# Performance work log

Measured on AMD Instinct MI355X. Metric: run time of the kernel, lower is better.

Reference implementation:

```python
import jax, jax.numpy as jnp
import numpy as np

N = 100000
NCLASS = 64
E = 1600000
NHID = 256
TOPK = 16
DEGREE = 9


def setup_inputs() -> dict:
    key = jax.random.key(0)
    ks = jax.random.split(key, 10)
    return {
        "f_prediction": jax.random.normal(ks[0], (N, NCLASS), dtype=jnp.float32),
        "g0_prediction": jax.random.normal(ks[1], (N, NCLASS), dtype=jnp.float32),
        "adj_rows": jax.random.randint(ks[2], (E,), 0, N, dtype=jnp.int32),
        "adj_cols": jax.random.randint(ks[3], (E,), 0, N, dtype=jnp.int32),
        "adj_vals": jax.random.uniform(ks[4], (E,), dtype=jnp.float32) / 16.0,
        "W1": jax.random.normal(ks[5], (TOPK, 2 * NHID), dtype=jnp.float32) * 0.1,
        "b1": jnp.zeros((2 * NHID,), dtype=jnp.float32),
        "W2": jax.random.normal(ks[6], (2 * NHID, NHID), dtype=jnp.float32) * 0.1,
        "b2": jnp.zeros((NHID,), dtype=jnp.float32),
        "W3": jax.random.normal(ks[7], (NHID, DEGREE), dtype=jnp.float32) * 0.1,
        "b3": jnp.zeros((DEGREE,), dtype=jnp.float32),
    }


def spmm(rows, cols, vals, x):
    # out[i] = sum_{e: rows[e]==i} vals[e] * x[cols[e]]
    msgs = vals[:, None] * x[cols]  # [E, F]
    return jax.ops.segment_sum(msgs, rows, num_segments=N)


def reference(f_prediction, g0_prediction, adj_rows, adj_cols, adj_vals,
              W1, b1, W2, b2, W3, b3):
    g0 = jax.nn.softmax(g0_prediction, axis=1)
    ranked, _ = jax.lax.top_k(g0, TOPK)  # [N, TOPK], sorted descending
    h = jnp.tanh(ranked @ W1 + b1)
    h = jnp.tanh(h @ W2 + b2)
    weight = h @ W3 + b3  # [N, DEGREE]

    f = f_prediction
    final = weight[:, 0:1] * f
    for i in range(DEGREE - 1):
        f = spmm(adj_rows, adj_cols, adj_vals, f)
        final = final + weight[:, i + 1:i + 2] * f
    return jax.nn.log_softmax(final, axis=1), weight
```

## Files before the change

### kernel.cpp

```cpp
#include <hip/hip_runtime.h>
#include <hip/hip_bf16.h>

#define N_NODES 100000
#define NCLASS  64
#define NEDGE   1600000
#define NHID    256
#define TOPK    16
#define DEGREE  9

#define TM 16
#define KCHUNK 128
#define H2PAD (NHID + 4)

__device__ __forceinline__ float fast_tanh(float x) {
    float e = __expf(2.0f * x);
    return 1.0f - 2.0f / (e + 1.0f);
}


__global__ void hist_kernel(const int* __restrict__ rows, int* __restrict__ counts, int e) {
    for (int i = blockIdx.x * blockDim.x + threadIdx.x; i < e; i += gridDim.x * blockDim.x)
        atomicAdd(&counts[rows[i]], 1);
}

__global__ __launch_bounds__(1024) void scan_blocks(const int* __restrict__ counts,
                                                    int* __restrict__ partial,
                                                    int* __restrict__ blocksums, int n) {
    __shared__ int s[1024];
    int tid = threadIdx.x;
    int gid = blockIdx.x * 1024 + tid;
    int v = (gid < n) ? counts[gid] : 0;
    s[tid] = v;
    __syncthreads();
    for (int off = 1; off < 1024; off <<= 1) {
        int t = (tid >= off) ? s[tid - off] : 0;
        __syncthreads();
        s[tid] += t;
        __syncthreads();
    }
    if (gid < n) partial[gid] = s[tid] - v;
    if (tid == 1023) blocksums[blockIdx.x] = s[1023];
}

__global__ void scan_sums(int* __restrict__ blocksums, int nb) {
    if (blockIdx.x == 0 && threadIdx.x == 0) {
        int run = 0;
        for (int i = 0; i < nb; ++i) { int v = blocksums[i]; blocksums[i] = run; run += v; }
    }
}

__global__ void finalize_rows(const int* __restrict__ partial, const int* __restrict__ blocksums,
                              int* __restrict__ row_start, int* __restrict__ cursor, int n, int e) {
    int i = blockIdx.x * blockDim.x + threadIdx.x;
    if (i < n) {
        int v = partial[i] + blocksums[i >> 10];
        row_start[i] = v;
        cursor[i] = v;
    }
    if (i == 0) row_start[n] = e;
}

__global__ void scatter_edges(const int* __restrict__ rows, const int* __restrict__ cols,
                              const float* __restrict__ vals, int* __restrict__ cursor,
                              int2* __restrict__ sedge, int e) {
    for (int i = blockIdx.x * blockDim.x + threadIdx.x; i < e; i += gridDim.x * blockDim.x) {
        int r = rows[i];
        int pos = atomicAdd(&cursor[r], 1);
        sedge[pos] = make_int2(cols[i], __float_as_int(vals[i]));
    }
}


__global__ __launch_bounds__(256) void softmax_topk(const float* __restrict__ g0,
                                                    float* __restrict__ ranked, int n) {
    int wave = (blockIdx.x * 256 + threadIdx.x) >> 6;
    int lane = threadIdx.x & 63;
    if (wave >= n) return;
    float x = g0[(size_t)wave * NCLASS + lane];
    float m = x;
    #pragma unroll
    for (int o = 1; o < 64; o <<= 1) m = fmaxf(m, __shfl_xor(m, o));
    float p = expf(x - m);
    float s = p;
    #pragma unroll
    for (int o = 1; o < 64; o <<= 1) s += __shfl_xor(s, o);
    p /= s;
    float v = p;
    #pragma unroll
    for (int k = 2; k <= 64; k <<= 1) {
        #pragma unroll
        for (int j = k >> 1; j > 0; j >>= 1) {
            float o = __shfl_xor(v, j);
            bool up = (lane & k) != 0;
            bool takeMax = (((lane & j) == 0) != up);
            v = takeMax ? fmaxf(v, o) : fminf(v, o);
        }
    }
    if (lane < TOPK) ranked[wave * TOPK + lane] = v;
}


__global__ __launch_bounds__(256) void mlp_kernel(const float* __restrict__ ranked,
                                                  const float* __restrict__ W1, const float* __restrict__ b1,
                                                  const float* __restrict__ W2, const float* __restrict__ b2,
                                                  const float* __restrict__ W3, const float* __restrict__ b3,
                                                  float* __restrict__ weight_out, int n) {
    __shared__ float s_rank[TM][TOPK];
    __shared__ float s_h1[TM][KCHUNK];
    __shared__ float s_h2[TM][H2PAD];
    int t = threadIdx.x;
    int row0 = blockIdx.x * TM;

    {
        int r = t >> 4, k = t & 15;
        int gr = row0 + r;
        s_rank[r][k] = (gr < n) ? ranked[gr * TOPK + k] : 0.0f;
    }

    const int tx = t & 63;
    const int ty = t >> 6;
    float acc[4][4];
    {
        float4 b2v = *reinterpret_cast<const float4*>(&b2[tx * 4]);
        #pragma unroll
        for (int rr = 0; rr < 4; ++rr) {
            acc[rr][0] = b2v.x; acc[rr][1] = b2v.y; acc[rr][2] = b2v.z; acc[rr][3] = b2v.w;
        }
    }
    const float* w2p = W2 + tx * 4;

    const int j  = t & (KCHUNK - 1);
    const int rh = (t >> 7) * 8;

    __syncthreads();

    for (int c = 0; c < 2 * NHID / KCHUNK; ++c) {
        const int kbase = c * KCHUNK;
        {
            const int col = kbase + j;
            float w1c[TOPK];
            #pragma unroll
            for (int k = 0; k < TOPK; ++k) w1c[k] = W1[k * (2 * NHID) + col];
            float bb = b1[col];
            #pragma unroll
            for (int r = rh; r < rh + 8; ++r) {
                float4 q0 = *reinterpret_cast<const float4*>(&s_rank[r][0]);
                float4 q1 = *reinterpret_cast<const float4*>(&s_rank[r][4]);
                float4 q2 = *reinterpret_cast<const float4*>(&s_rank[r][8]);
                float4 q3 = *reinterpret_cast<const float4*>(&s_rank[r][12]);
                float rk[TOPK] = {q0.x, q0.y, q0.z, q0.w, q1.x, q1.y, q1.z, q1.w,
                                  q2.x, q2.y, q2.z, q2.w, q3.x, q3.y, q3.z, q3.w};
                float a = bb;
                #pragma unroll
                for (int k = 0; k < TOPK; ++k) a = fmaf(rk[k], w1c[k], a);
                s_h1[r][j] = fast_tanh(a);
            }
        }
        __syncthreads();

        for (int kk = 0; kk < KCHUNK; kk += 4) {
            float4 h[4];
            #pragma unroll
            for (int rr = 0; rr < 4; ++rr)
                h[rr] = *reinterpret_cast<const float4*>(&s_h1[ty * 4 + rr][kk]);
            #pragma unroll
            for (int kk2 = 0; kk2 < 4; ++kk2) {
                float4 w = *reinterpret_cast<const float4*>(&w2p[(size_t)(kbase + kk + kk2) * NHID]);
                #pragma unroll
                for (int rr = 0; rr < 4; ++rr) {
                    float hv = (kk2 == 0) ? h[rr].x : (kk2 == 1) ? h[rr].y : (kk2 == 2) ? h[rr].z : h[rr].w;
                    acc[rr][0] = fmaf(hv, w.x, acc[rr][0]);
                    acc[rr][1] = fmaf(hv, w.y, acc[rr][1]);
                    acc[rr][2] = fmaf(hv, w.z, acc[rr][2]);
                    acc[rr][3] = fmaf(hv, w.w, acc[rr][3]);
                }
            }
        }
        __syncthreads();
    }

    #pragma unroll
    for (int rr = 0; rr < 4; ++rr) {
        #pragma unroll
        for (int cc = 0; cc < 4; ++cc)
            s_h2[ty * 4 + rr][tx * 4 + cc] = fast_tanh(acc[rr][cc]);
    }
    __syncthreads();

    if (t < TM * DEGREE) {
        int r = t / DEGREE, d = t % DEGREE;
        float a3 = b3[d];
        for (int k = 0; k < NHID; k += 4) {
            float4 h = *reinterpret_cast<const float4*>(&s_h2[r][k]);
            a3 = fmaf(h.x, W3[(k + 0) * DEGREE + d], a3);
            a3 = fmaf(h.y, W3[(k + 1) * DEGREE + d], a3);
            a3 = fmaf(h.z, W3[(k + 2) * DEGREE + d], a3);
            a3 = fmaf(h.w, W3[(k + 3) * DEGREE + d], a3);
        }
        int gr = row0 + r;
        if (gr < n) weight_out[gr * DEGREE + d] = a3;
    }
}


__global__ void init_final(const float* __restrict__ fpred, const float* __restrict__ weight,
                           float* __restrict__ finalbuf, int n) {
    int i = blockIdx.x * blockDim.x + threadIdx.x;
    if (i < n * NCLASS) {
        int row = i >> 6;
        finalbuf[i] = weight[row * DEGREE] * fpred[i];
    }
}

__global__ __launch_bounds__(256) void spmm_fused(const int* __restrict__ row_start,
                                                  const int2* __restrict__ sedge,
                                                  const float* __restrict__ x,
                                                  float* __restrict__ y,
                                                  const float* __restrict__ weight,
                                                  float* __restrict__ finalbuf,
                                                  int wcol, int n) {
    int wave = (blockIdx.x * 256 + threadIdx.x) >> 6;
    int lane = threadIdx.x & 63;
    if (wave >= n) return;
    int e0 = row_start[wave], e1 = row_start[wave + 1];
    float a0 = 0.0f, a1 = 0.0f, a2 = 0.0f, a3 = 0.0f;
    int e = e0;
    for (; e + 3 < e1; e += 4) {
        int2 d0 = sedge[e];
        int2 d1 = sedge[e + 1];
        int2 d2 = sedge[e + 2];
        int2 d3 = sedge[e + 3];
        float x0 = x[(size_t)d0.x * NCLASS + lane];
        float x1 = x[(size_t)d1.x * NCLASS + lane];
        float x2 = x[(size_t)d2.x * NCLASS + lane];
        float x3 = x[(size_t)d3.x * NCLASS + lane];
        a0 = fmaf(__int_as_float(d0.y), x0, a0);
        a1 = fmaf(__int_as_float(d1.y), x1, a1);
        a2 = fmaf(__int_as_float(d2.y), x2, a2);
        a3 = fmaf(__int_as_float(d3.y), x3, a3);
    }
    for (; e < e1; ++e) {
        int2 d = sedge[e];
        a0 = fmaf(__int_as_float(d.y), x[(size_t)d.x * NCLASS + lane], a0);
    }
    float acc = (a0 + a1) + (a2 + a3);
    int o = wave * NCLASS + lane;
    y[o] = acc;
    finalbuf[o] += weight[wave * DEGREE + wcol] * acc;
}

__global__ __launch_bounds__(256) void logsoftmax_inplace(float* __restrict__ out, int n) {
    int wave = (blockIdx.x * 256 + threadIdx.x) >> 6;
    int lane = threadIdx.x & 63;
    if (wave >= n) return;
    int o = wave * NCLASS + lane;
    float x = out[o];
    float m = x;
    #pragma unroll
    for (int off = 1; off < 64; off <<= 1) m = fmaxf(m, __shfl_xor(m, off));
    float p = expf(x - m);
    float s = p;
    #pragma unroll
    for (int off = 1; off < 64; off <<= 1) s += __shfl_xor(s, off);
    out[o] = x - m - logf(s);
}


extern "C" void kernel_launch(void* const* d_in, const int* in_sizes, int n_in,
                              void* d_out, int out_size, void* d_ws, size_t ws_size,
                              hipStream_t stream) {
    const float* f_pred = (const float*)d_in[0];
    const float* g0     = (const float*)d_in[1];
    const int*   arows  = (const int*)d_in[2];
    const int*   acols  = (const int*)d_in[3];
    const float* avals  = (const float*)d_in[4];
    const float* W1     = (const float*)d_in[5];
    const float* b1     = (const float*)d_in[6];
    const float* W2     = (const float*)d_in[7];
    const float* b2     = (const float*)d_in[8];
    const float* W3     = (const float*)d_in[9];
    const float* b3     = (const float*)d_in[10];

    float* out_ls = (float*)d_out;
    float* weight = (float*)d_out + (size_t)N_NODES * NCLASS;

    char* ws = (char*)d_ws;
    size_t off = 0;
    auto alloc = [&](size_t bytes) {
        void* p = ws + off;
        off += (bytes + 255) & ~(size_t)255;
        return p;
    };
    float* ranked    = (float*)alloc((size_t)N_NODES * TOPK * 4);
    float* fA        = (float*)alloc((size_t)N_NODES * NCLASS * 4);
    float* fB        = (float*)alloc((size_t)N_NODES * NCLASS * 4);
    int*   counts    = (int*)alloc((size_t)N_NODES * 4);
    int*   partial   = (int*)alloc((size_t)N_NODES * 4);
    int*   row_start = (int*)alloc((size_t)(N_NODES + 1) * 4);
    int*   cursor    = (int*)alloc((size_t)N_NODES * 4);
    int*   blocksums = (int*)alloc(128 * 4);
    int2*  sedge     = (int2*)alloc((size_t)NEDGE * 8);

    const int SCAN_BLOCKS = (N_NODES + 1023) / 1024;

    hipMemsetAsync(counts, 0, (size_t)N_NODES * 4, stream);
    hist_kernel<<<2048, 256, 0, stream>>>(arows, counts, NEDGE);
    scan_blocks<<<SCAN_BLOCKS, 1024, 0, stream>>>(counts, partial, blocksums, N_NODES);
    scan_sums<<<1, 64, 0, stream>>>(blocksums, SCAN_BLOCKS);
    finalize_rows<<<(N_NODES + 255) / 256, 256, 0, stream>>>(partial, blocksums, row_start, cursor,
                                                             N_NODES, NEDGE);
    scatter_edges<<<2048, 256, 0, stream>>>(arows, acols, avals, cursor, sedge, NEDGE);

    softmax_topk<<<(N_NODES + 3) / 4, 256, 0, stream>>>(g0, ranked, N_NODES);
    mlp_kernel<<<(N_NODES + TM - 1) / TM, 256, 0, stream>>>(ranked, W1, b1, W2, b2, W3, b3,
                                                            weight, N_NODES);

    init_final<<<(N_NODES * NCLASS + 255) / 256, 256, 0, stream>>>(f_pred, weight, out_ls, N_NODES);

    const float* xin = f_pred;
    float* bufs[2] = {fA, fB};
    for (int it = 0; it < DEGREE - 1; ++it) {
        float* y = bufs[it & 1];
        spmm_fused<<<(N_NODES + 3) / 4, 256, 0, stream>>>(row_start, sedge, xin, y, weight, out_ls,
                                                          it + 1, N_NODES);
        xin = y;
    }

    logsoftmax_inplace<<<(N_NODES + 3) / 4, 256, 0, stream>>>(out_ls, N_NODES);
}
```

Before: 1.516 ms.

## Enlarge MLP row tile, prefetch W2 rows, and unroll SpMM gather by eight

Result: faster. 1.377 ms (-9.2%).

```diff
diff --git a/kernel.cpp b/kernel.cpp
--- a/kernel.cpp
+++ b/kernel.cpp
@@ -8,7 +8,7 @@
 #define TOPK    16
 #define DEGREE  9
 
-#define TM 16
+#define TM 32
 #define KCHUNK 128
 #define H2PAD (NHID + 4)
 
@@ -111,26 +111,25 @@
     int t = threadIdx.x;
     int row0 = blockIdx.x * TM;
 
-    {
-        int r = t >> 4, k = t & 15;
+    for (int idx = t; idx < TM * TOPK; idx += 256) {
+        int r = idx >> 4, k = idx & 15;
         int gr = row0 + r;
         s_rank[r][k] = (gr < n) ? ranked[gr * TOPK + k] : 0.0f;
     }
 
     const int tx = t & 63;
     const int ty = t >> 6;
-    float acc[4][4];
+    float acc[8][4];
     {
         float4 b2v = *reinterpret_cast<const float4*>(&b2[tx * 4]);
         #pragma unroll
-        for (int rr = 0; rr < 4; ++rr) {
+        for (int rr = 0; rr < 8; ++rr) {
             acc[rr][0] = b2v.x; acc[rr][1] = b2v.y; acc[rr][2] = b2v.z; acc[rr][3] = b2v.w;
         }
     }
-    const float* w2p = W2 + tx * 4;
 
     const int j  = t & (KCHUNK - 1);
-    const int rh = (t >> 7) * 8;
+    const int rh = (t >> 7) * (TM / 2);
 
     __syncthreads();
 
@@ -142,8 +141,8 @@
             #pragma unroll
             for (int k = 0; k < TOPK; ++k) w1c[k] = W1[k * (2 * NHID) + col];
             float bb = b1[col];
-            #pragma unroll
-            for (int r = rh; r < rh + 8; ++r) {
+            #pragma unroll 4
+            for (int r = rh; r < rh + TM / 2; ++r) {
                 float4 q0 = *reinterpret_cast<const float4*>(&s_rank[r][0]);
                 float4 q1 = *reinterpret_cast<const float4*>(&s_rank[r][4]);
                 float4 q2 = *reinterpret_cast<const float4*>(&s_rank[r][8]);
@@ -158,21 +157,38 @@
         }
         __syncthreads();
 
-        for (int kk = 0; kk < KCHUNK; kk += 4) {
-            float4 h[4];
-            #pragma unroll
-            for (int rr = 0; rr < 4; ++rr)
-                h[rr] = *reinterpret_cast<const float4*>(&s_h1[ty * 4 + rr][kk]);
-            #pragma unroll
-            for (int kk2 = 0; kk2 < 4; ++kk2) {
-                float4 w = *reinterpret_cast<const float4*>(&w2p[(size_t)(kbase + kk + kk2) * NHID]);
+        {
+            const float* wk = W2 + (size_t)kbase * NHID + (tx << 2);
+            float4 wa0 = *reinterpret_cast<const float4*>(wk);
+            float4 wa1 = *reinterpret_cast<const float4*>(wk + NHID);
+            float4 wa2 = *reinterpret_cast<const float4*>(wk + 2 * NHID);
+            float4 wa3 = *reinterpret_cast<const float4*>(wk + 3 * NHID);
+            wk += 4 * NHID;
+            for (int kk = 0; kk < KCHUNK; kk += 4) {
+                float4 w0 = wa0, w1 = wa1, w2v = wa2, w3v = wa3;
+                if (kk + 4 < KCHUNK) {
+                    wa0 = *reinterpret_cast<const float4*>(wk);
+                    wa1 = *reinterpret_cast<const float4*>(wk + NHID);
+                    wa2 = *reinterpret_cast<const float4*>(wk + 2 * NHID);
+                    wa3 = *reinterpret_cast<const float4*>(wk + 3 * NHID);
+                    wk += 4 * NHID;
+                }
+                float4 h[8];
                 #pragma unroll
-                for (int rr = 0; rr < 4; ++rr) {
-                    float hv = (kk2 == 0) ? h[rr].x : (kk2 == 1) ? h[rr].y : (kk2 == 2) ? h[rr].z : h[rr].w;
-                    acc[rr][0] = fmaf(hv, w.x, acc[rr][0]);
-                    acc[rr][1] = fmaf(hv, w.y, acc[rr][1]);
-                    acc[rr][2] = fmaf(hv, w.z, acc[rr][2]);
-                    acc[rr][3] = fmaf(hv, w.w, acc[rr][3]);
+                for (int rr = 0; rr < 8; ++rr)
+                    h[rr] = *reinterpret_cast<const float4*>(&s_h1[ty * 8 + rr][kk]);
+                #pragma unroll
+                for (int kk2 = 0; kk2 < 4; ++kk2) {
+                    float4 w = (kk2 == 0) ? w0 : (kk2 == 1) ? w1 : (kk2 == 2) ? w2v : w3v;
+                    #pragma unroll
+                    for (int rr = 0; rr < 8; ++rr) {
+                        float hv = (kk2 == 0) ? h[rr].x : (kk2 == 1) ? h[rr].y
+                                 : (kk2 == 2) ? h[rr].z : h[rr].w;
+                        acc[rr][0] = fmaf(hv, w.x, acc[rr][0]);
+                        acc[rr][1] = fmaf(hv, w.y, acc[rr][1]);
+                        acc[rr][2] = fmaf(hv, w.z, acc[rr][2]);
+                        acc[rr][3] = fmaf(hv, w.w, acc[rr][3]);
+                    }
                 }
             }
         }
@@ -180,15 +196,15 @@
     }
 
     #pragma unroll
-    for (int rr = 0; rr < 4; ++rr) {
+    for (int rr = 0; rr < 8; ++rr) {
         #pragma unroll
         for (int cc = 0; cc < 4; ++cc)
-            s_h2[ty * 4 + rr][tx * 4 + cc] = fast_tanh(acc[rr][cc]);
+            s_h2[ty * 8 + rr][tx * 4 + cc] = fast_tanh(acc[rr][cc]);
     }
     __syncthreads();
 
-    if (t < TM * DEGREE) {
-        int r = t / DEGREE, d = t % DEGREE;
+    for (int idx = t; idx < TM * DEGREE; idx += 256) {
+        int r = idx / DEGREE, d = idx % DEGREE;
         float a3 = b3[d];
         for (int k = 0; k < NHID; k += 4) {
             float4 h = *reinterpret_cast<const float4*>(&s_h2[r][k]);
@@ -224,7 +240,34 @@
     if (wave >= n) return;
     int e0 = row_start[wave], e1 = row_start[wave + 1];
     float a0 = 0.0f, a1 = 0.0f, a2 = 0.0f, a3 = 0.0f;
+    float a4 = 0.0f, a5 = 0.0f, a6 = 0.0f, a7 = 0.0f;
     int e = e0;
+    for (; e + 7 < e1; e += 8) {
+        int2 d0 = sedge[e];
+        int2 d1 = sedge[e + 1];
+        int2 d2 = sedge[e + 2];
+        int2 d3 = sedge[e + 3];
+        int2 d4 = sedge[e + 4];
+        int2 d5 = sedge[e + 5];
+        int2 d6 = sedge[e + 6];
+        int2 d7 = sedge[e + 7];
+        float x0 = x[(size_t)d0.x * NCLASS + lane];
+        float x1 = x[(size_t)d1.x * NCLASS + lane];
+        float x2 = x[(size_t)d2.x * NCLASS + lane];
+        float x3 = x[(size_t)d3.x * NCLASS + lane];
+        float x4 = x[(size_t)d4.x * NCLASS + lane];
+        float x5 = x[(size_t)d5.x * NCLASS + lane];
+        float x6 = x[(size_t)d6.x * NCLASS + lane];
+        float x7 = x[(size_t)d7.x * NCLASS + lane];
+        a0 = fmaf(__int_as_float(d0.y), x0, a0);
+        a1 = fmaf(__int_as_float(d1.y), x1, a1);
+        a2 = fmaf(__int_as_float(d2.y), x2, a2);
+        a3 = fmaf(__int_as_float(d3.y), x3, a3);
+        a4 = fmaf(__int_as_float(d4.y), x4, a4);
+        a5 = fmaf(__int_as_float(d5.y), x5, a5);
+        a6 = fmaf(__int_as_float(d6.y), x6, a6);
+        a7 = fmaf(__int_as_float(d7.y), x7, a7);
+    }
     for (; e + 3 < e1; e += 4) {
         int2 d0 = sedge[e];
         int2 d1 = sedge[e + 1];
@@ -243,7 +286,7 @@
         int2 d = sedge[e];
         a0 = fmaf(__int_as_float(d.y), x[(size_t)d.x * NCLASS + lane], a0);
     }
-    float acc = (a0 + a1) + (a2 + a3);
+    float acc = ((a0 + a1) + (a2 + a3)) + ((a4 + a5) + (a6 + a7));
     int o = wave * NCLASS + lane;
     y[o] = acc;
     finalbuf[o] += weight[wave * DEGREE + wcol] * acc;
```
